# Optimization experiments

Hardware: AMD Instinct MI355X
Metric: run time of the kernel (lower is better)

Reference implementation:

```python
import jax, jax.numpy as jnp
import numpy as np

# hypercfg constants (init_kwargs)
AUX = 0.05
L1W = 5.0
VPW = 1.0
VNW = 1.0


def _lsa_square(cost):
    """Jonker-Volgenant shortest-augmenting-path Hungarian on a square numpy
    cost matrix. Returns rows[j] = row assigned to column j. Runs on host,
    mirroring the original CPU scipy.optimize.linear_sum_assignment call."""
    n = cost.shape[0]
    INF = np.inf
    u = np.zeros(n + 1)
    v = np.zeros(n + 1)
    p = np.zeros(n + 1, dtype=np.int64)   # p[j] = row matched to column j (1-indexed)
    way = np.zeros(n + 1, dtype=np.int64)
    for i in range(1, n + 1):
        p[0] = i
        j0 = 0
        minv = np.full(n + 1, INF)
        used = np.zeros(n + 1, dtype=bool)
        while True:
            used[j0] = True
            i0 = p[j0]
            cur = cost[i0 - 1, :] - u[i0] - v[1:]
            free = ~used[1:]
            upd = free & (cur < minv[1:])
            minv1 = minv[1:]
            minv1[upd] = cur[upd]
            way1 = way[1:]
            way1[upd] = j0
            mfree = np.where(free, minv1, INF)
            j1 = int(np.argmin(mfree)) + 1
            delta = mfree[j1 - 1]
            used_idx = np.nonzero(used)[0]
            u[p[used_idx]] += delta
            v[used_idx] -= delta
            minv1[free] -= delta
            j0 = j1
            if p[j0] == 0:
                break
        while j0 != 0:
            j1 = way[j0]
            p[j0] = p[j1]
            j0 = j1
    return p[1:] - 1


def _match(cost_mk):
    """Rectangular assignment, cost [M, K] with K <= M: pad with a constant
    column block (dummy columns cost the same for any row, so the real K
    columns get the optimal assignment, matching scipy on rectangles)."""
    M, K = cost_mk.shape
    pad = np.zeros((M, M), dtype=np.float64)
    pad[:, :K] = cost_mk
    rows = _lsa_square(pad)
    return rows[:K]


def _cost(meta_points, meta_visibles, gtpoints, gtvisibles):
    # meta_points: [S,B,L,M,2]  gtpoints: [S,B,K,2]
    # meta_visibles: [S,B,M,1]  gtvisibles: [S,B,K,1]
    S, B, L, M, _ = meta_points.shape
    # pairwise L1 cost: [S,B,L,M,K]
    diff = jnp.abs(meta_points[:, :, :, :, None, :] - gtpoints[:, :, None, None, :, :]).sum(-1)
    # delta[l] = L - (l+1), per-layer slack (torch.linspace(1, L, L))
    delta = (L - jnp.arange(1, L + 1, dtype=meta_points.dtype)) * AUX
    cost_p_ml = jax.nn.relu(diff - delta[None, None, :, None, None])
    gtv = gtvisibles[:, :, :, 0][:, :, None, :]          # [S,B,1,K]
    cost_p = gtv * cost_p_ml.mean(2)                     # [S,B,M,K]
    cost_vp = -gtv * jnp.log(meta_visibles)              # [S,B,M,1] -> [S,B,M,K]
    cost_vn = -(1.0 - gtv) * jnp.log(1.0 - meta_visibles)
    cost = L1W * cost_p + VPW * cost_vp + VNW * cost_vn  # [S,B,M,K]
    return cost.mean(0)                                  # mean over shots -> [B,M,K]


def setup_inputs() -> dict:
    key = jax.random.key(0)
    ks = jax.random.split(key, 5)
    S, B, L, M, K = 6, 16, 8, 256, 128
    meta_points = jax.random.uniform(ks[0], (S, B, L, M, 2), dtype=jnp.float32)
    # keep probabilities strictly inside (0,1) so log() is finite
    meta_visibles = jax.random.uniform(ks[1], (S, B, M, 1), dtype=jnp.float32) * 0.9 + 0.05
    covisibles = jax.random.uniform(ks[2], (B, K), dtype=jnp.float32)
    gtpoints = jax.random.uniform(ks[3], (S, B, K, 2), dtype=jnp.float32)
    gtvisibles = (jax.random.uniform(ks[4], (S, B, K, 1)) > 0.5).astype(jnp.float32)
    return {
        "meta_points": meta_points,
        "meta_visibles": meta_visibles,
        "covisibles": covisibles,
        "gtpoints": gtpoints,
        "gtvisibles": gtvisibles,
    }


def reference(meta_points, meta_visibles, covisibles, gtpoints, gtvisibles):
    # covisibles only provides the batch size in the original module
    cost = np.asarray(jax.jit(_cost)(meta_points, meta_visibles, gtpoints, gtvisibles))
    bs = cost.shape[0]
    # per-batch Hungarian on host (sequential data-dependent algorithm);
    # result[b, k] = meta index matched to keypoint k (already kp-sorted,
    # matching the argsort-reorder in the torch code)
    out = np.stack([_match(cost[b]) for b in range(bs)])
    return jnp.asarray(out, dtype=jnp.int64)
```

## Files before the change

kernel.cpp:

```cpp
#include <hip/hip_runtime.h>
#include <math.h>


#define S_ 6
#define B_ 16
#define L_ 8
#define M_ 256
#define K_ 128

__global__ void cost_kernel(const float* __restrict__ mp,
                            const float* __restrict__ mv,
                            const float* __restrict__ gt,
                            const float* __restrict__ gv,
                            float* __restrict__ cost)
{
#pragma clang fp contract(off)
    const int b = blockIdx.x;
    const int m = blockIdx.y;
    const int k = threadIdx.x;

    float accS = 0.0f;
    for (int s = 0; s < S_; ++s) {
        const int sb = s * B_ + b;
        const float gx = gt[(sb * K_ + k) * 2 + 0];
        const float gy = gt[(sb * K_ + k) * 2 + 1];
        float accL = 0.0f;
#pragma unroll
        for (int l = 0; l < L_; ++l) {
            const int base = ((sb * L_ + l) * M_ + m) * 2;
            const float dx = fabsf(mp[base + 0] - gx);
            const float dy = fabsf(mp[base + 1] - gy);
            const float diff = dx + dy;
            const float dl = (float)(L_ - (l + 1)) * 0.05f;
            const float t = diff - dl;
            accL += fmaxf(t, 0.0f);
        }
        const float meanL = accL * 0.125f;
        const float mvv = mv[sb * M_ + m];
        const float gtv = gv[sb * K_ + k];
        const float lp = -logf(mvv);
        const float ln = -logf(1.0f - mvv);
        const float val = (gtv != 0.0f) ? (5.0f * meanL + lp) : ln;
        accS += val;
    }
    cost[(b * M_ + m) * K_ + k] = accS * (1.0f / 6.0f);
}

__device__ __forceinline__ double bits2d(int lo, int hi) {
    const unsigned long long u =
        ((unsigned long long)(unsigned)hi << 32) | (unsigned)lo;
    return __longlong_as_double((long long)u);
}
__device__ __forceinline__ void d2bits(double d, int& lo, int& hi) {
    const unsigned long long u = (unsigned long long)__double_as_longlong(d);
    lo = (int)(u & 0xffffffffull);
    hi = (int)(u >> 32);
}
__device__ __forceinline__ double readlane_d(double d, int l) {
    int lo, hi; d2bits(d, lo, hi);
    return bits2d(__builtin_amdgcn_readlane(lo, l),
                  __builtin_amdgcn_readlane(hi, l));
}

#define RSTG(LOV, HIV, FOP, CTRL, RM)                                            \
    {                                                                            \
        const int nlo_ = __builtin_amdgcn_update_dpp(LOV, LOV, CTRL, RM, 0xf, false); \
        const int nhi_ = __builtin_amdgcn_update_dpp(HIV, HIV, CTRL, RM, 0xf, false); \
        const double r_ = FOP(bits2d(LOV, HIV), bits2d(nlo_, nhi_));             \
        d2bits(r_, LOV, HIV);                                                    \
    }
#define RLADDER(LOV, HIV, FOP)                                                   \
    RSTG(LOV, HIV, FOP, 0x111, 0xf)                              \
    RSTG(LOV, HIV, FOP, 0x112, 0xf)                              \
    RSTG(LOV, HIV, FOP, 0x114, 0xf)                              \
    RSTG(LOV, HIV, FOP, 0x118, 0xf)                              \
    RSTG(LOV, HIV, FOP, 0x142, 0xa)                \
    RSTG(LOV, HIV, FOP, 0x143, 0xc)

__global__ __launch_bounds__(64, 1) void match_kernel(const float* __restrict__ cost,
                                                      int* __restrict__ out)
{
#pragma clang fp contract(off)
    const int b = blockIdx.x;
    const int lane = threadIdx.x;
    const float* C = cost + (size_t)b * M_ * K_;
    const double INF = __builtin_inf();
    const double NINF = -__builtin_inf();
    const int BIG = 0x7fffffff;

    __shared__ float  C_lds[M_ * K_];
    __shared__ double u_lds[257];
    __shared__ int    p_lds[257];

    for (int t = lane; t < (M_ * K_) / 4; t += 64)
        ((float4*)C_lds)[t] = ((const float4*)C)[t];

    for (int t = lane; t < 257; t += 64) {
        u_lds[t] = 0.0;
        p_lds[t] = (t >= 129) ? (t - 128) : 0;
    }
    __syncthreads();

    double v0 = 0.0, v1 = 0.0, v2 = 0.0, v3 = 0.0;
    const int jd2 = 2 * lane + 129;
    const int jd3 = 2 * lane + 130;

    int jdC = 129; double vdC = 0.0, udC = 0.0;

    for (int i = 129; i <= 256; ++i) {
        const int pj0 = p_lds[2 * lane + 1];
        const int pj1 = p_lds[2 * lane + 2];
        double ur0 = u_lds[pj0], ur1 = u_lds[pj1];
        double ur2 = u_lds[2 * lane + 1], ur3 = u_lds[2 * lane + 2];
        const double up0 = ur0, up1 = ur1, up2 = ur2, up3 = ur3;

        float2 cc = *(const float2*)(C_lds + (i - 1) * K_ + 2 * lane);
        double u_i0 = 0.0;
        int used = 0;
        int j1 = 0;
        double usum = 0.0;

        for (;;) {
            const float2 ccs = *(const float2*)(C_lds + (jdC - 129) * K_ + 2 * lane);
            const double dval = (0.0 - u_i0) - vdC;

            double cd0 = ((double)cc.x - u_i0) - v0;
            double cd1 = ((double)cc.y - u_i0) - v1;
            if (used & 1) cd0 = INF;
            if (used & 2) cd1 = INF;
            double bv = fmin(cd0, cd1);

            int lo, hi; d2bits(bv, lo, hi);
            RLADDER(lo, hi, fmin)
            const int mlo = __builtin_amdgcn_readlane(lo, 63);
            const int mhi = __builtin_amdgcn_readlane(hi, 63);
            const double rmin = bits2d(mlo, mhi);

            const double vm2 = ((used & 4) || (jd2 == jdC)) ? NINF : v2;
            const double vm3 = ((used & 8) || (jd3 == jdC)) ? NINF : v3;
            double bx = fmax(vm2, vm3);
            int xlo, xhi; d2bits(bx, xlo, xhi);
            RLADDER(xlo, xhi, fmax)
            const double vdN = bits2d(__builtin_amdgcn_readlane(xlo, 63),
                                      __builtin_amdgcn_readlane(xhi, 63));
            int jc = BIG;
            if (vm3 == vdN) jc = jd3;
            if (vm2 == vdN) jc = jd2;
            const unsigned long long bd = __ballot(jc != BIG);
            const int jdN = __builtin_amdgcn_readlane(jc, (int)__builtin_ctzll(bd));
            const int olN = (jdN - 129) >> 1, slN = (jdN - 129) & 1;
            const double udN = readlane_d(slN ? up3 : up2, olN);

            if (rmin <= dval) {
                const double delta = rmin;
                int jr = BIG;
                if (cd1 == delta) jr = 2 * lane + 2;
                if (cd0 == delta) jr = 2 * lane + 1;
                const unsigned long long br = __ballot(jr != BIG);
                j1 = __builtin_amdgcn_readlane(jr, (int)__builtin_ctzll(br));

                const int ol = (j1 - 1) >> 1, sl = (j1 - 1) & 1;
                const int psel = sl ? pj1 : pj0;
                const int i0n = __builtin_amdgcn_readlane(psel, ol);

                const int rown = (i0n > 0 ? i0n : 1) - 1;
                const float2 ccn = *(const float2*)(C_lds + rown * K_ + 2 * lane);

                usum += delta;
                if (used & 1) { ur0 += delta; v0 -= delta; }
                if (used & 2) { ur1 += delta; v1 -= delta; }
                if (used & 4) { ur2 += delta; v2 -= delta; }
                if (used & 8) { ur3 += delta; v3 -= delta; }

                const double u_n = readlane_d(sl ? up1 : up0, ol);

                if (i0n == 0) break;
                if (lane == ol) used |= (1 << sl);
                u_i0 = u_n;
                cc = ccn;
            } else {
                const double delta = dval;
                usum += delta;
                if (used & 1) { ur0 += delta; v0 -= delta; }
                if (used & 2) { ur1 += delta; v1 -= delta; }
                if (used & 4) { ur2 += delta; v2 -= delta; }
                if (used & 8) { ur3 += delta; v3 -= delta; }

                j1 = jdC;
                const int olc = (jdC - 129) >> 1, slc = (jdC - 129) & 1;
                if (lane == olc) used |= (4 << slc);
                u_i0 = udC;
                cc = ccs;
                jdC = jdN; vdC = vdN; udC = udN;
            }
        }

        __syncthreads();
        if (used & 1) u_lds[pj0] = ur0;
        if (used & 2) u_lds[pj1] = ur1;
        if (used & 4) u_lds[2 * lane + 1] = ur2;
        if (used & 8) u_lds[2 * lane + 2] = ur3;
        if (lane == 0) { p_lds[j1] = i; u_lds[i] = usum; }

        {
            double bx = fmax(v2, v3);
            int xlo, xhi; d2bits(bx, xlo, xhi);
            RLADDER(xlo, xhi, fmax)
            vdC = bits2d(__builtin_amdgcn_readlane(xlo, 63),
                         __builtin_amdgcn_readlane(xhi, 63));
            int jc = BIG;
            if (v3 == vdC) jc = jd3;
            if (v2 == vdC) jc = jd2;
            const unsigned long long bd = __ballot(jc != BIG);
            jdC = __builtin_amdgcn_readlane(jc, (int)__builtin_ctzll(bd));
            const int olc = (jdC - 129) >> 1, slc = (jdC - 129) & 1;
            udC = readlane_d(slc ? ur3 : ur2, olc);
        }
        __syncthreads();
    }

    for (int j = lane; j < K_; j += 64)
        out[b * K_ + j] = p_lds[j + 1] - 1;
}

extern "C" void kernel_launch(void* const* d_in, const int* in_sizes, int n_in,
                              void* d_out, int out_size, void* d_ws, size_t ws_size,
                              hipStream_t stream) {
    const float* mp = (const float*)d_in[0];
    const float* mv = (const float*)d_in[1];
    const float* gt = (const float*)d_in[3];
    const float* gv = (const float*)d_in[4];
    int* out = (int*)d_out;
    float* cost = (float*)d_ws;

    dim3 gridA(B_, M_);
    cost_kernel<<<gridA, K_, 0, stream>>>(mp, mv, gt, gv, cost);
    match_kernel<<<B_, 64, 0, stream>>>(cost, out);
}
```

Baseline: 1.485 ms.

## Pipeline dummy-column selection two ahead and defer dummy potential updates

The matching loop keeps a two-deep lookahead queue (head and next) of dummy columns, with their costs prefetched from LDS. This takes the dummy-column argmax reduction off the critical dependency of each step. Dummy-column v/u updates are no longer applied in registers at every step. Instead they are logged with the cumulative delta and applied lazily after each row augmentation, using the difference from the final sum. This removes per-step work and the end-of-row re-selection, at the cost of more LDS traffic and more complex bookkeeping that could diverge numerically from the reference.

Measured after the change: 1.644 ms. +10.7%, slower.

```diff
diff --git a/kernel.cpp b/kernel.cpp
--- a/kernel.cpp
+++ b/kernel.cpp
@@ -77,6 +77,26 @@
     RSTG(LOV, HIV, FOP, 0x142, 0xa)                \
     RSTG(LOV, HIV, FOP, 0x143, 0xc)
 
+#define SELBEST(EXJ1, EXJ2, JOUT, VOUT, UOUT)                                    \
+    {                                                                            \
+        const double vm2_ = ((used & 4) || (jd2 == (EXJ1)) || (jd2 == (EXJ2)))   \
+                                ? NINF : v2;                                     \
+        const double vm3_ = ((used & 8) || (jd3 == (EXJ1)) || (jd3 == (EXJ2)))   \
+                                ? NINF : v3;                                     \
+        const double bx_ = fmax(vm2_, vm3_);                                     \
+        int xlo_, xhi_; d2bits(bx_, xlo_, xhi_);                                 \
+        RLADDER(xlo_, xhi_, fmax)                                                \
+        VOUT = bits2d(__builtin_amdgcn_readlane(xlo_, 63),                       \
+                      __builtin_amdgcn_readlane(xhi_, 63));                      \
+        int jc_ = BIG;                                                           \
+        if (vm3_ == VOUT) jc_ = jd3;                                             \
+        if (vm2_ == VOUT) jc_ = jd2;               \
+        const unsigned long long bd_ = __ballot(jc_ != BIG);                     \
+        JOUT = __builtin_amdgcn_readlane(jc_, (int)__builtin_ctzll(bd_));        \
+        const int ol_ = ((JOUT) - 129) >> 1, sl_ = ((JOUT) - 129) & 1;           \
+        UOUT = readlane_d(sl_ ? up3 : up2, ol_);                                 \
+    }
+
 __global__ __launch_bounds__(64, 1) void match_kernel(const float* __restrict__ cost,
                                                       int* __restrict__ out)
 {
@@ -91,6 +111,9 @@
     __shared__ float  C_lds[M_ * K_];
     __shared__ double u_lds[257];
     __shared__ int    p_lds[257];
+    __shared__ double vd_lds[128];
+    __shared__ double Dcons[128];
+    __shared__ int    clog[128];
 
     for (int t = lane; t < (M_ * K_) / 4; t += 64)
         ((float4*)C_lds)[t] = ((const float4*)C)[t];
@@ -99,60 +122,57 @@
         u_lds[t] = 0.0;
         p_lds[t] = (t >= 129) ? (t - 128) : 0;
     }
+    for (int t = lane; t < 128; t += 64) vd_lds[t] = 0.0;
     __syncthreads();
 
-    double v0 = 0.0, v1 = 0.0, v2 = 0.0, v3 = 0.0;
+    double v0 = 0.0, v1 = 0.0;
     const int jd2 = 2 * lane + 129;
     const int jd3 = 2 * lane + 130;
-
-    int jdC = 129; double vdC = 0.0, udC = 0.0;
 
     for (int i = 129; i <= 256; ++i) {
         const int pj0 = p_lds[2 * lane + 1];
         const int pj1 = p_lds[2 * lane + 2];
         double ur0 = u_lds[pj0], ur1 = u_lds[pj1];
-        double ur2 = u_lds[2 * lane + 1], ur3 = u_lds[2 * lane + 2];
-        const double up0 = ur0, up1 = ur1, up2 = ur2, up3 = ur3;
+        const double up0 = ur0, up1 = ur1;
+        const double up2 = u_lds[2 * lane + 1];
+        const double up3 = u_lds[2 * lane + 2];
+        const double v2 = vd_lds[2 * lane];
+        const double v3 = vd_lds[2 * lane + 1];
 
         float2 cc = *(const float2*)(C_lds + (i - 1) * K_ + 2 * lane);
         double u_i0 = 0.0;
         int used = 0;
+        double usum = 0.0;
         int j1 = 0;
-        double usum = 0.0;
+        int ptr = 0;
+
+        int jdH, jdQ, jdN; double vdH, vdQ, vdN, udH, udQ, udN;
+        SELBEST(-1, -1, jdH, vdH, udH)
+        SELBEST(jdH, -1, jdQ, vdQ, udQ)
+        float2 ccH = *(const float2*)(C_lds + (jdH - 129) * K_ + 2 * lane);
+        float2 ccQ = *(const float2*)(C_lds + (jdQ - 129) * K_ + 2 * lane);
+        double dval = (0.0 - u_i0) - vdH;
 
         for (;;) {
-            const float2 ccs = *(const float2*)(C_lds + (jdC - 129) * K_ + 2 * lane);
-            const double dval = (0.0 - u_i0) - vdC;
-
             double cd0 = ((double)cc.x - u_i0) - v0;
             double cd1 = ((double)cc.y - u_i0) - v1;
             if (used & 1) cd0 = INF;
             if (used & 2) cd1 = INF;
             double bv = fmin(cd0, cd1);
-
             int lo, hi; d2bits(bv, lo, hi);
             RLADDER(lo, hi, fmin)
-            const int mlo = __builtin_amdgcn_readlane(lo, 63);
-            const int mhi = __builtin_amdgcn_readlane(hi, 63);
-            const double rmin = bits2d(mlo, mhi);
-
-            const double vm2 = ((used & 4) || (jd2 == jdC)) ? NINF : v2;
-            const double vm3 = ((used & 8) || (jd3 == jdC)) ? NINF : v3;
-            double bx = fmax(vm2, vm3);
-            int xlo, xhi; d2bits(bx, xlo, xhi);
-            RLADDER(xlo, xhi, fmax)
-            const double vdN = bits2d(__builtin_amdgcn_readlane(xlo, 63),
-                                      __builtin_amdgcn_readlane(xhi, 63));
-            int jc = BIG;
-            if (vm3 == vdN) jc = jd3;
-            if (vm2 == vdN) jc = jd2;
-            const unsigned long long bd = __ballot(jc != BIG);
-            const int jdN = __builtin_amdgcn_readlane(jc, (int)__builtin_ctzll(bd));
-            const int olN = (jdN - 129) >> 1, slN = (jdN - 129) & 1;
-            const double udN = readlane_d(slN ? up3 : up2, olN);
+            const double rmin = bits2d(__builtin_amdgcn_readlane(lo, 63),
+                                       __builtin_amdgcn_readlane(hi, 63));
+
+            SELBEST(jdH, jdQ, jdN, vdN, udN)
+            const float2 ccN = *(const float2*)(C_lds + (jdN - 129) * K_ + 2 * lane);
 
             if (rmin <= dval) {
                 const double delta = rmin;
+                usum += delta;
+                if (used & 1) { ur0 += delta; v0 -= delta; }
+                if (used & 2) { ur1 += delta; v1 -= delta; }
+
                 int jr = BIG;
                 if (cd1 == delta) jr = 2 * lane + 2;
                 if (cd0 == delta) jr = 2 * lane + 1;
@@ -162,60 +182,50 @@
                 const int ol = (j1 - 1) >> 1, sl = (j1 - 1) & 1;
                 const int psel = sl ? pj1 : pj0;
                 const int i0n = __builtin_amdgcn_readlane(psel, ol);
-
-                const int rown = (i0n > 0 ? i0n : 1) - 1;
-                const float2 ccn = *(const float2*)(C_lds + rown * K_ + 2 * lane);
-
-                usum += delta;
-                if (used & 1) { ur0 += delta; v0 -= delta; }
-                if (used & 2) { ur1 += delta; v1 -= delta; }
-                if (used & 4) { ur2 += delta; v2 -= delta; }
-                if (used & 8) { ur3 += delta; v3 -= delta; }
+                if (i0n == 0) break;
 
                 const double u_n = readlane_d(sl ? up1 : up0, ol);
-
-                if (i0n == 0) break;
                 if (lane == ol) used |= (1 << sl);
                 u_i0 = u_n;
-                cc = ccn;
+                cc = *(const float2*)(C_lds + (i0n - 1) * K_ + 2 * lane);
+                dval = (0.0 - u_i0) - vdH;
             } else {
                 const double delta = dval;
                 usum += delta;
                 if (used & 1) { ur0 += delta; v0 -= delta; }
                 if (used & 2) { ur1 += delta; v1 -= delta; }
-                if (used & 4) { ur2 += delta; v2 -= delta; }
-                if (used & 8) { ur3 += delta; v3 -= delta; }
-
-                j1 = jdC;
-                const int olc = (jdC - 129) >> 1, slc = (jdC - 129) & 1;
+                if (lane == 0) { clog[ptr] = jdH; Dcons[ptr] = usum; }
+                ++ptr;
+                const int olc = (jdH - 129) >> 1, slc = (jdH - 129) & 1;
                 if (lane == olc) used |= (4 << slc);
-                u_i0 = udC;
-                cc = ccs;
-                jdC = jdN; vdC = vdN; udC = udN;
+                j1 = jdH;
+                u_i0 = udH;
+                cc = ccH;
+                jdH = jdQ; vdH = vdQ; udH = udQ; ccH = ccQ;
+                jdQ = jdN; vdQ = vdN; udQ = udN; ccQ = ccN;
+                dval = (0.0 - u_i0) - vdH;
             }
         }
 
         __syncthreads();
         if (used & 1) u_lds[pj0] = ur0;
         if (used & 2) u_lds[pj1] = ur1;
-        if (used & 4) u_lds[2 * lane + 1] = ur2;
-        if (used & 8) u_lds[2 * lane + 2] = ur3;
+        {
+            const int t0 = 2 * lane, t1 = 2 * lane + 1;
+            if (t0 < ptr) {
+                const int j = clog[t0];
+                const double amt = usum - Dcons[t0];
+                u_lds[j - 128] += amt;
+                vd_lds[j - 129] -= amt;
+            }
+            if (t1 < ptr) {
+                const int j = clog[t1];
+                const double amt = usum - Dcons[t1];
+                u_lds[j - 128] += amt;
+                vd_lds[j - 129] -= amt;
+            }
+        }
         if (lane == 0) { p_lds[j1] = i; u_lds[i] = usum; }
-
-        {
-            double bx = fmax(v2, v3);
-            int xlo, xhi; d2bits(bx, xlo, xhi);
-            RLADDER(xlo, xhi, fmax)
-            vdC = bits2d(__builtin_amdgcn_readlane(xlo, 63),
-                         __builtin_amdgcn_readlane(xhi, 63));
-            int jc = BIG;
-            if (v3 == vdC) jc = jd3;
-            if (v2 == vdC) jc = jd2;
-            const unsigned long long bd = __ballot(jc != BIG);
-            jdC = __builtin_amdgcn_readlane(jc, (int)__builtin_ctzll(bd));
-            const int olc = (jdC - 129) >> 1, slc = (jdC - 129) & 1;
-            udC = readlane_d(slc ? ur3 : ur2, olc);
-        }
         __syncthreads();
     }
 
```
